# Kernel optimization log

Measured on AMD Instinct MI355X. Metric: run time of the kernel, lower is better.

Reference implementation:

```python
import jax, jax.numpy as jnp
import numpy as np

NUM_LEVELS = 4
RADIUS = 4


def avg_pool2(x):
    # x: [N, H, W] -> [N, H//2, W//2] (kernel 2, stride 2 average pool)
    n, h, w = x.shape
    return x.reshape(n, h // 2, 2, w // 2, 2).mean(axis=(2, 4))


def bilinear_sample(img, x, y):
    # img: [N, H, W]; x, y: [N, S, S] absolute pixel coords (align_corners=True),
    # zero padding outside [0, W-1] x [0, H-1] (matches F.grid_sample defaults).
    n, h, w = img.shape
    x0 = jnp.floor(x)
    y0 = jnp.floor(y)
    wx1 = x - x0
    wy1 = y - y0
    wx0 = 1.0 - wx1
    wy0 = 1.0 - wy1
    nidx = jnp.arange(n)[:, None, None]

    def gather(yi, xi):
        valid = (xi >= 0) & (xi <= w - 1) & (yi >= 0) & (yi <= h - 1)
        xic = jnp.clip(xi, 0, w - 1).astype(jnp.int32)
        yic = jnp.clip(yi, 0, h - 1).astype(jnp.int32)
        return jnp.where(valid, img[nidx, yic, xic], 0.0)

    return (gather(y0, x0) * wy0 * wx0 + gather(y0, x0 + 1) * wy0 * wx1
            + gather(y0 + 1, x0) * wy1 * wx0 + gather(y0 + 1, x0 + 1) * wy1 * wx1)


def setup_inputs() -> dict:
    key = jax.random.key(0)
    k1, k2, k3 = jax.random.split(key, 3)
    b, c, h, w = 2, 256, 64, 64
    fmap1 = jax.random.normal(k1, (b, c, h, w), dtype=jnp.float32)
    fmap2 = jax.random.normal(k2, (b, c, h, w), dtype=jnp.float32)
    # absolute pixel (x, y) coordinates in [0, W-1] / [0, H-1]
    centroids_coords = jax.random.uniform(k3, (b, 2, h, w), dtype=jnp.float32) * (w - 1)
    return {"fmap1": fmap1, "fmap2": fmap2, "centroids_coords": centroids_coords}


def reference(fmap1, fmap2, centroids_coords):
    b, c, h1, w1 = fmap1.shape
    h2, w2 = fmap2.shape[-2:]
    # correlation volume: [b, h1*w1, h2*w2] / sqrt(c)
    f1 = fmap1.reshape(b, c, h1 * w1)
    f2 = fmap2.reshape(b, c, h2 * w2)
    corr = jnp.einsum('bcm,bcn->bmn', f1, f2) / jnp.sqrt(jnp.asarray(c, fmap1.dtype))
    corr = corr.reshape(b * h1 * w1, h2, w2)

    pyramid = [corr]
    for _ in range(NUM_LEVELS - 1):
        corr = avg_pool2(corr)
        pyramid.append(corr)

    side = 2 * RADIUS + 1
    di = jnp.linspace(-RADIUS, RADIUS, side)
    # delta[..., 0] = di (added to x), delta[..., 1] = dj (added to y) -- as in source
    delta = jnp.stack(jnp.meshgrid(di, di, indexing='ij'), axis=-1)  # [S, S, 2]

    cc = centroids_coords.transpose(0, 2, 3, 1).reshape(b * h1 * w1, 1, 1, 2)
    feats = []
    for lvl, vol in enumerate(pyramid):
        grid = cc / (2.0 ** lvl) + delta[None]  # [N, S, S, 2]
        sampled = bilinear_sample(vol, grid[..., 0], grid[..., 1])  # [N, S, S]
        feats.append(sampled.reshape(b, h1, w1, side * side))
    # [b, num_levels*side^2, h1, w1]
    return jnp.concatenate(feats, axis=-1).transpose(0, 3, 1, 2)
```

## Files before the change

### kernel.cpp

```cpp
#include <hip/hip_runtime.h>
#include <stdint.h>

#define M_DIM 4096
#define K_DIM 256

typedef unsigned short us;
typedef __attribute__((ext_vector_type(8))) short bf16x8;
typedef __attribute__((ext_vector_type(4))) float f32x4;

static __device__ __forceinline__ float bf2f(unsigned int u){
  unsigned int x = u << 16; float f;
  __builtin_memcpy(&f, &x, 4); return f;
}
static __device__ __forceinline__ us f2bf(float f){
  unsigned int x; __builtin_memcpy(&x, &f, 4);
  unsigned int r = x + 0x7fffu + ((x >> 16) & 1u);
  return (us)(r >> 16);
}
static __device__ __forceinline__ void gld16(const void* g, void* l){
  __builtin_amdgcn_global_load_lds(
      (const __attribute__((address_space(1))) unsigned int*)g,
      (__attribute__((address_space(3))) unsigned int*)l, 16, 0, 0);
}

__global__ void k_transpose_cast(const float* __restrict__ f1,
                                 const float* __restrict__ f2,
                                 us* __restrict__ A, us* __restrict__ B0){
  __shared__ float lds[64][65];
  int z = blockIdx.z;
  int b = z & 1, which = z >> 1;
  const float* in = which ? f2 : f1;
  us* out = which ? B0 : A;
  float scale = which ? 1.0f : 0.0625f;
  int c0 = blockIdx.y * 64, m0 = blockIdx.x * 64;
  const float* ib = in + (size_t)b * K_DIM * M_DIM;
  us* ob = out + (size_t)b * M_DIM * K_DIM;
  int t = threadIdx.x, r = t >> 6, j = t & 63;
#pragma unroll
  for (int k = 0; k < 16; k++)
    lds[r + k*4][j] = ib[(size_t)(c0 + r + k*4) * M_DIM + m0 + j];
  __syncthreads();
#pragma unroll
  for (int k = 0; k < 16; k++)
    ob[(size_t)(m0 + r + k*4) * K_DIM + c0 + j] = f2bf(lds[j][r + k*4] * scale);
}

__global__ void k_pool_all(const us* __restrict__ B0, us* __restrict__ B1,
                           us* __restrict__ B2, us* __restrict__ B3){
  int bid = blockIdx.x;
  us* dst; int wd, f;
  if (bid < 512)      { dst = B1; wd = 32; f = 2; }
  else if (bid < 640) { bid -= 512; dst = B2; wd = 16; f = 4; }
  else                { bid -= 640; dst = B3; wd = 8;  f = 8; }
  int t = threadIdx.x;
  int idx = bid * 4 + (t >> 6);
  int l = t & 63;
  int per = wd * wd;
  int b = idx / per, rem = idx - b * per;
  int y = rem / wd, x = rem - y * wd;
  const us* sb = B0 + (size_t)b * 4096 * K_DIM;
  float s0 = 0, s1 = 0, s2 = 0, s3 = 0;
  for (int dy = 0; dy < f; dy++)
    for (int dx = 0; dx < f; dx++){
      size_t off = ((size_t)(f*y + dy) * 64 + (f*x + dx)) * K_DIM + l * 4;
      uint2 v = *(const uint2*)(sb + off);
      s0 += bf2f(v.x & 0xffff); s1 += bf2f(v.x >> 16);
      s2 += bf2f(v.y & 0xffff); s3 += bf2f(v.y >> 16);
    }
  float inv = 1.0f / (float)(f * f);
  uint2 o;
  o.x = (unsigned)f2bf(s0*inv) | ((unsigned)f2bf(s1*inv) << 16);
  o.y = (unsigned)f2bf(s2*inv) | ((unsigned)f2bf(s3*inv) << 16);
  us* db = dst + (size_t)b * per * K_DIM;
  *(uint2*)(db + (size_t)rem * K_DIM + l * 4) = o;
}

__global__ __launch_bounds__(256) void k_gemm_all(
    const us* __restrict__ A,
    const us* __restrict__ B0, const us* __restrict__ B1,
    const us* __restrict__ B2, const us* __restrict__ B3,
    us* __restrict__ C0, us* __restrict__ C1,
    us* __restrict__ C2, us* __restrict__ C3){
  __shared__ __align__(16) us As[2][4096];
  __shared__ __align__(16) us Bs[2][4096];
  int bx = blockIdx.x;
  const us* B; us* C; int N, n0;
  if (bx < 32)      { B = B0; C = C0; N = 4096; n0 = bx * 128; }
  else if (bx < 40) { B = B1; C = C1; N = 1024; n0 = (bx - 32) * 128; }
  else if (bx < 42) { B = B2; C = C2; N = 256;  n0 = (bx - 40) * 128; }
  else              { B = B3; C = C3; N = 64;   n0 = 0; }
  int b = blockIdx.z;
  const us* Ab = A + (size_t)b * M_DIM * K_DIM;
  const us* Bb = B + (size_t)b * N * K_DIM;
  us* Cb = C + (size_t)b * M_DIM * N;
  int m0 = blockIdx.y * 128;
  int t = threadIdx.x;
  int wave = t >> 6, lane = t & 63;
  int wm = (wave >> 1) * 64, wn = (wave & 1) * 64;
  int srow = t >> 2, scol = (t & 3) * 8;
  int fr = lane & 15, fk = (lane >> 4) * 8;
  f32x4 acc[4][4];
#pragma unroll
  for (int i = 0; i < 4; i++)
#pragma unroll
    for (int j = 0; j < 4; j++) acc[i][j] = (f32x4){0.f, 0.f, 0.f, 0.f};

  int nr0 = n0 + srow;      if (nr0 > N - 1) nr0 = N - 1;
  int nr1 = n0 + srow + 64; if (nr1 > N - 1) nr1 = N - 1;
  const us* ga0 = Ab + (size_t)(m0 + srow) * K_DIM + scol;
  const us* ga1 = Ab + (size_t)(m0 + srow + 64) * K_DIM + scol;
  const us* gb0 = Bb + (size_t)nr0 * K_DIM + scol;
  const us* gb1 = Bb + (size_t)nr1 * K_DIM + scol;

  gld16(ga0, &As[0][t*8]);
  gld16(ga1, &As[0][t*8 + 2048]);
  gld16(gb0, &Bs[0][t*8]);
  gld16(gb1, &Bs[0][t*8 + 2048]);
  asm volatile("s_waitcnt vmcnt(0)" ::: "memory");
  __syncthreads();

  int cur = 0;
  for (int it = 0; it < 8; ++it){
    if (it < 7){
      int kt = (it + 1) * 32;
      gld16(ga0 + kt, &As[cur^1][t*8]);
      gld16(ga1 + kt, &As[cur^1][t*8 + 2048]);
      gld16(gb0 + kt, &Bs[cur^1][t*8]);
      gld16(gb1 + kt, &Bs[cur^1][t*8 + 2048]);
    }
    bf16x8 af[4], bfv[4];
#pragma unroll
    for (int i = 0; i < 4; i++)
      af[i] = *(const bf16x8*)&As[cur][(wm + i*16 + fr) * 32 + fk];
#pragma unroll
    for (int j = 0; j < 4; j++)
      bfv[j] = *(const bf16x8*)&Bs[cur][(wn + j*16 + fr) * 32 + fk];
#pragma unroll
    for (int i = 0; i < 4; i++)
#pragma unroll
      for (int j = 0; j < 4; j++)
        acc[i][j] = __builtin_amdgcn_mfma_f32_16x16x32_bf16(af[i], bfv[j], acc[i][j], 0, 0, 0);
    asm volatile("s_waitcnt vmcnt(0)" ::: "memory");
    __syncthreads();
    cur ^= 1;
  }

  int cr = (lane >> 4) * 4, ccol = lane & 15;
#pragma unroll
  for (int i = 0; i < 4; i++){
#pragma unroll
    for (int j = 0; j < 4; j++){
      int col = n0 + wn + j*16 + ccol;
      if (col < N){
        size_t base = (size_t)(m0 + wm + i*16 + cr) * N + col;
#pragma unroll
        for (int r = 0; r < 4; r++)
          Cb[base + (size_t)r * N] = f2bf(acc[i][j][r]);
      }
    }
  }
}

__global__ __launch_bounds__(512) void k_sample(
    const us* __restrict__ p0, const us* __restrict__ p1,
    const us* __restrict__ p2, const us* __restrict__ p3,
    const float* __restrict__ cc, float* __restrict__ out){
  int i = blockIdx.x, b = blockIdx.y, lvl = blockIdx.z;
  int t = threadIdx.x;
  int w = t >> 6, j = t & 63;
  const us* corr; int wl;
  if (lvl == 0)      { corr = p0; wl = 64; }
  else if (lvl == 1) { corr = p1; wl = 32; }
  else if (lvl == 2) { corr = p2; wl = 16; }
  else               { corr = p3; wl = 8;  }
  float inv = 1.0f / (float)(1 << lvl);
  int m = i * 64 + j;
  const us* rowp = corr + (size_t)(b * M_DIM + m) * (wl * wl);
  float cx = cc[((size_t)(b*2 + 0) * 64 + i) * 64 + j];
  float cy = cc[((size_t)(b*2 + 1) * 64 + i) * 64 + j];
  float x = cx * inv, y = cy * inv;
  float x0f = floorf(x), y0f = floorf(y);
  int x0 = (int)x0f, y0 = (int)y0f;
  float fx = x - x0f, fy = y - y0f;

  int d_lo  = (w == 0) ? 0 : w + 1;
  int d_cnt = (w == 0) ? 2 : 1;
  int nrows = d_cnt + 1;

  int bxi = x0 - 4;
  int a0 = bxi & ~1;
  int par = bxi & 1;

  float Cw[3][12];
#pragma unroll
  for (int v = 0; v < 3; v++){
    int ry = y0 - 4 + d_lo + v;
    bool vy = ((unsigned)ry < (unsigned)wl) && (v < nrows);
    int ryc = ry < 0 ? 0 : (ry > wl - 1 ? wl - 1 : ry);
    const us* rp = rowp + ryc * wl;
#pragma unroll
    for (int k = 0; k < 6; k++){
      int e = a0 + 2*k;
      int ec = e < 0 ? 0 : (e > wl - 2 ? wl - 2 : e);
      unsigned dv = *(const unsigned*)(rp + ec);
      Cw[v][2*k]   = vy ? bf2f(dv & 0xffff) : 0.0f;
      Cw[v][2*k+1] = vy ? bf2f(dv >> 16)    : 0.0f;
    }
  }
  float T[3][10];
#pragma unroll
  for (int v = 0; v < 3; v++)
#pragma unroll
    for (int u = 0; u < 10; u++){
      float val = par ? Cw[v][u+1] : Cw[v][u];
      bool vx = (unsigned)(bxi + u) < (unsigned)wl;
      T[v][u] = vx ? val : 0.0f;
    }

  float wx1 = fx, wx0 = 1.0f - fx, wy1 = fy, wy0 = 1.0f - fy;
  size_t ob = (size_t)b * 324 + lvl * 81;
#pragma unroll
  for (int dd = 0; dd < 2; dd++){
    if (dd < d_cnt){
      int d = d_lo + dd;
#pragma unroll
      for (int a = 0; a < 9; a++){
        float val = wy0 * (wx0 * T[dd][a]   + wx1 * T[dd][a+1])
                  + wy1 * (wx0 * T[dd+1][a] + wx1 * T[dd+1][a+1]);
        out[((ob + a*9 + d) * 64 + i) * 64 + j] = val;
      }
    }
  }
}

extern "C" void kernel_launch(void* const* d_in, const int* in_sizes, int n_in,
                              void* d_out, int out_size, void* d_ws, size_t ws_size,
                              hipStream_t stream){
  (void)in_sizes; (void)n_in; (void)out_size; (void)ws_size;
  const float* f1 = (const float*)d_in[0];
  const float* f2 = (const float*)d_in[1];
  const float* cc = (const float*)d_in[2];
  float* out = (float*)d_out;
  char* ws = (char*)d_ws;
  us* A  = (us*)(ws + 0);
  us* B0 = (us*)(ws + 4194304);
  us* B1 = (us*)(ws + 8388608);
  us* B2 = (us*)(ws + 9437184);
  us* B3 = (us*)(ws + 9699328);
  us* C0 = (us*)(ws + 9764864);
  us* C1 = (us*)(ws + 76873728);
  us* C2 = (us*)(ws + 93650944);
  us* C3 = (us*)(ws + 97845248);

  k_transpose_cast<<<dim3(64, 4, 4), dim3(256), 0, stream>>>(f1, f2, A, B0);
  k_pool_all<<<dim3(672), dim3(256), 0, stream>>>(B0, B1, B2, B3);
  k_gemm_all<<<dim3(43, 32, 2), dim3(256), 0, stream>>>(A, B0, B1, B2, B3, C0, C1, C2, C3);
  k_sample<<<dim3(64, 2, 4), dim3(512), 0, stream>>>(C0, C1, C2, C3, cc, out);
}
```

Baseline: 160.7 us.

## Compute only the sampled correlation windows instead of the full correlation volume

Replaces the full all-pairs correlation GEMM and the separate sampling kernel with one fused kernel. Each wave handles one pixel and one pyramid level. It uses MFMA to compute dot products between that pixel's fmap1 feature and only the 10x10 neighbourhood of pooled fmap2 features, then does the bilinear interpolation from LDS. This relies on average pooling commuting with the dot product. It removes the large GEMM and the write and read of the tens-of-megabytes bf16 correlation volume. In exchange it does scattered row gathers from the pooled fmap2 buffers, and only one MFMA column out of sixteen is useful.

```diff
diff --git a/kernel.cpp b/kernel.cpp
--- a/kernel.cpp
+++ b/kernel.cpp
@@ -16,11 +16,6 @@
   unsigned int x; __builtin_memcpy(&x, &f, 4);
   unsigned int r = x + 0x7fffu + ((x >> 16) & 1u);
   return (us)(r >> 16);
-}
-static __device__ __forceinline__ void gld16(const void* g, void* l){
-  __builtin_amdgcn_global_load_lds(
-      (const __attribute__((address_space(1))) unsigned int*)g,
-      (__attribute__((address_space(3))) unsigned int*)l, 16, 0, 0);
 }
 
 __global__ void k_transpose_cast(const float* __restrict__ f1,
@@ -75,160 +70,82 @@
   *(uint2*)(db + (size_t)rem * K_DIM + l * 4) = o;
 }
 
-__global__ __launch_bounds__(256) void k_gemm_all(
+__global__ __launch_bounds__(256) void k_corrsample(
     const us* __restrict__ A,
     const us* __restrict__ B0, const us* __restrict__ B1,
     const us* __restrict__ B2, const us* __restrict__ B3,
-    us* __restrict__ C0, us* __restrict__ C1,
-    us* __restrict__ C2, us* __restrict__ C3){
-  __shared__ __align__(16) us As[2][4096];
-  __shared__ __align__(16) us Bs[2][4096];
-  int bx = blockIdx.x;
-  const us* B; us* C; int N, n0;
-  if (bx < 32)      { B = B0; C = C0; N = 4096; n0 = bx * 128; }
-  else if (bx < 40) { B = B1; C = C1; N = 1024; n0 = (bx - 32) * 128; }
-  else if (bx < 42) { B = B2; C = C2; N = 256;  n0 = (bx - 40) * 128; }
-  else              { B = B3; C = C3; N = 64;   n0 = 0; }
-  int b = blockIdx.z;
-  const us* Ab = A + (size_t)b * M_DIM * K_DIM;
-  const us* Bb = B + (size_t)b * N * K_DIM;
-  us* Cb = C + (size_t)b * M_DIM * N;
-  int m0 = blockIdx.y * 128;
-  int t = threadIdx.x;
-  int wave = t >> 6, lane = t & 63;
-  int wm = (wave >> 1) * 64, wn = (wave & 1) * 64;
-  int srow = t >> 2, scol = (t & 3) * 8;
-  int fr = lane & 15, fk = (lane >> 4) * 8;
-  f32x4 acc[4][4];
+    const float* __restrict__ cc, float* __restrict__ out){
+  __shared__ float tlds[4][112];
+  int wv = threadIdx.x >> 6, lane = threadIdx.x & 63;
+  int px = blockIdx.x;
+  int lvl = wv;
+  int b = px >> 12, m = px & 4095;
+  int i = m >> 6, j = m & 63;
+
+  const us* Bl; int wl;
+  if (lvl == 0)      { Bl = B0 + (size_t)b * 4096 * K_DIM; wl = 64; }
+  else if (lvl == 1) { Bl = B1 + (size_t)b * 1024 * K_DIM; wl = 32; }
+  else if (lvl == 2) { Bl = B2 + (size_t)b * 256  * K_DIM; wl = 16; }
+  else               { Bl = B3 + (size_t)b * 64   * K_DIM; wl = 8;  }
+  float inv = (lvl == 0) ? 1.0f : (lvl == 1) ? 0.5f : (lvl == 2) ? 0.25f : 0.125f;
+
+  float cx = cc[((size_t)(b*2 + 0) * 64 + i) * 64 + j];
+  float cy = cc[((size_t)(b*2 + 1) * 64 + i) * 64 + j];
+  float xs = cx * inv, ys = cy * inv;
+  float x0f = floorf(xs), y0f = floorf(ys);
+  int bx0 = (int)x0f - 4, by0 = (int)y0f - 4;
+  float fx = xs - x0f, fy = ys - y0f;
+
+  const us* f1p = A + (size_t)px * K_DIM;
+  int ko = (lane >> 4) * 8;
+  bf16x8 fB[8];
 #pragma unroll
-  for (int i = 0; i < 4; i++)
+  for (int kk = 0; kk < 8; kk++)
+    fB[kk] = *(const bf16x8*)(f1p + kk*32 + ko);
+
 #pragma unroll
-    for (int j = 0; j < 4; j++) acc[i][j] = (f32x4){0.f, 0.f, 0.f, 0.f};
-
-  int nr0 = n0 + srow;      if (nr0 > N - 1) nr0 = N - 1;
-  int nr1 = n0 + srow + 64; if (nr1 > N - 1) nr1 = N - 1;
-  const us* ga0 = Ab + (size_t)(m0 + srow) * K_DIM + scol;
-  const us* ga1 = Ab + (size_t)(m0 + srow + 64) * K_DIM + scol;
-  const us* gb0 = Bb + (size_t)nr0 * K_DIM + scol;
-  const us* gb1 = Bb + (size_t)nr1 * K_DIM + scol;
-
-  gld16(ga0, &As[0][t*8]);
-  gld16(ga1, &As[0][t*8 + 2048]);
-  gld16(gb0, &Bs[0][t*8]);
-  gld16(gb1, &Bs[0][t*8 + 2048]);
-  asm volatile("s_waitcnt vmcnt(0)" ::: "memory");
-  __syncthreads();
-
-  int cur = 0;
-  for (int it = 0; it < 8; ++it){
-    if (it < 7){
-      int kt = (it + 1) * 32;
-      gld16(ga0 + kt, &As[cur^1][t*8]);
-      gld16(ga1 + kt, &As[cur^1][t*8 + 2048]);
-      gld16(gb0 + kt, &Bs[cur^1][t*8]);
-      gld16(gb1 + kt, &Bs[cur^1][t*8 + 2048]);
+  for (int g = 0; g < 7; g++){
+    int tt = g*16 + (lane & 15);
+    int vv = (tt * 205) >> 11;
+    int uu = tt - vv * 10;
+    int ry = by0 + vv, rx = bx0 + uu;
+    int ryc = ry < 0 ? 0 : (ry > wl-1 ? wl-1 : ry);
+    int rxc = rx < 0 ? 0 : (rx > wl-1 ? wl-1 : rx);
+    const us* rowp = Bl + (size_t)(ryc * wl + rxc) * K_DIM;
+    f32x4 acc = (f32x4){0.f, 0.f, 0.f, 0.f};
+#pragma unroll
+    for (int kk = 0; kk < 8; kk++){
+      bf16x8 fA = *(const bf16x8*)(rowp + kk*32 + ko);
+      acc = __builtin_amdgcn_mfma_f32_16x16x32_bf16(fA, fB[kk], acc, 0, 0, 0);
     }
-    bf16x8 af[4], bfv[4];
+    int rbase = (lane >> 4) * 4;
+    float vals[4];
 #pragma unroll
-    for (int i = 0; i < 4; i++)
-      af[i] = *(const bf16x8*)&As[cur][(wm + i*16 + fr) * 32 + fk];
-#pragma unroll
-    for (int j = 0; j < 4; j++)
-      bfv[j] = *(const bf16x8*)&Bs[cur][(wn + j*16 + fr) * 32 + fk];
-#pragma unroll
-    for (int i = 0; i < 4; i++)
-#pragma unroll
-      for (int j = 0; j < 4; j++)
-        acc[i][j] = __builtin_amdgcn_mfma_f32_16x16x32_bf16(af[i], bfv[j], acc[i][j], 0, 0, 0);
-    asm volatile("s_waitcnt vmcnt(0)" ::: "memory");
-    __syncthreads();
-    cur ^= 1;
+    for (int rr = 0; rr < 4; rr++){
+      int tr = g*16 + rbase + rr;
+      int vr = (tr * 205) >> 11;
+      int ur = tr - vr * 10;
+      int ryr = by0 + vr, rxr = bx0 + ur;
+      bool ok = ((unsigned)ryr < (unsigned)wl) && ((unsigned)rxr < (unsigned)wl)
+                && (tr < 100);
+      vals[rr] = ok ? acc[rr] : 0.0f;
+    }
+    if ((lane & 15) == 0){
+      float4 v4; v4.x = vals[0]; v4.y = vals[1]; v4.z = vals[2]; v4.w = vals[3];
+      *(float4*)&tlds[wv][g*16 + rbase] = v4;
+    }
   }
 
-  int cr = (lane >> 4) * 4, ccol = lane & 15;
+  float wx1 = fx, wx0 = 1.0f - fx, wy1 = fy, wy0 = 1.0f - fy;
 #pragma unroll
-  for (int i = 0; i < 4; i++){
-#pragma unroll
-    for (int j = 0; j < 4; j++){
-      int col = n0 + wn + j*16 + ccol;
-      if (col < N){
-        size_t base = (size_t)(m0 + wm + i*16 + cr) * N + col;
-#pragma unroll
-        for (int r = 0; r < 4; r++)
-          Cb[base + (size_t)r * N] = f2bf(acc[i][j][r]);
-      }
-    }
-  }
-}
-
-__global__ __launch_bounds__(512) void k_sample(
-    const us* __restrict__ p0, const us* __restrict__ p1,
-    const us* __restrict__ p2, const us* __restrict__ p3,
-    const float* __restrict__ cc, float* __restrict__ out){
-  int i = blockIdx.x, b = blockIdx.y, lvl = blockIdx.z;
-  int t = threadIdx.x;
-  int w = t >> 6, j = t & 63;
-  const us* corr; int wl;
-  if (lvl == 0)      { corr = p0; wl = 64; }
-  else if (lvl == 1) { corr = p1; wl = 32; }
-  else if (lvl == 2) { corr = p2; wl = 16; }
-  else               { corr = p3; wl = 8;  }
-  float inv = 1.0f / (float)(1 << lvl);
-  int m = i * 64 + j;
-  const us* rowp = corr + (size_t)(b * M_DIM + m) * (wl * wl);
-  float cx = cc[((size_t)(b*2 + 0) * 64 + i) * 64 + j];
-  float cy = cc[((size_t)(b*2 + 1) * 64 + i) * 64 + j];
-  float x = cx * inv, y = cy * inv;
-  float x0f = floorf(x), y0f = floorf(y);
-  int x0 = (int)x0f, y0 = (int)y0f;
-  float fx = x - x0f, fy = y - y0f;
-
-  int d_lo  = (w == 0) ? 0 : w + 1;
-  int d_cnt = (w == 0) ? 2 : 1;
-  int nrows = d_cnt + 1;
-
-  int bxi = x0 - 4;
-  int a0 = bxi & ~1;
-  int par = bxi & 1;
-
-  float Cw[3][12];
-#pragma unroll
-  for (int v = 0; v < 3; v++){
-    int ry = y0 - 4 + d_lo + v;
-    bool vy = ((unsigned)ry < (unsigned)wl) && (v < nrows);
-    int ryc = ry < 0 ? 0 : (ry > wl - 1 ? wl - 1 : ry);
-    const us* rp = rowp + ryc * wl;
-#pragma unroll
-    for (int k = 0; k < 6; k++){
-      int e = a0 + 2*k;
-      int ec = e < 0 ? 0 : (e > wl - 2 ? wl - 2 : e);
-      unsigned dv = *(const unsigned*)(rp + ec);
-      Cw[v][2*k]   = vy ? bf2f(dv & 0xffff) : 0.0f;
-      Cw[v][2*k+1] = vy ? bf2f(dv >> 16)    : 0.0f;
-    }
-  }
-  float T[3][10];
-#pragma unroll
-  for (int v = 0; v < 3; v++)
-#pragma unroll
-    for (int u = 0; u < 10; u++){
-      float val = par ? Cw[v][u+1] : Cw[v][u];
-      bool vx = (unsigned)(bxi + u) < (unsigned)wl;
-      T[v][u] = vx ? val : 0.0f;
-    }
-
-  float wx1 = fx, wx0 = 1.0f - fx, wy1 = fy, wy0 = 1.0f - fy;
-  size_t ob = (size_t)b * 324 + lvl * 81;
-#pragma unroll
-  for (int dd = 0; dd < 2; dd++){
-    if (dd < d_cnt){
-      int d = d_lo + dd;
-#pragma unroll
-      for (int a = 0; a < 9; a++){
-        float val = wy0 * (wx0 * T[dd][a]   + wx1 * T[dd][a+1])
-                  + wy1 * (wx0 * T[dd+1][a] + wx1 * T[dd+1][a+1]);
-        out[((ob + a*9 + d) * 64 + i) * 64 + j] = val;
-      }
+  for (int rep = 0; rep < 2; rep++){
+    int o = lane + rep * 64;
+    if (o < 81){
+      int a = o / 9, d = o - a * 9;
+      int t0 = d * 10 + a;
+      float s = wy0 * (wx0 * tlds[wv][t0]      + wx1 * tlds[wv][t0 + 1])
+              + wy1 * (wx0 * tlds[wv][t0 + 10] + wx1 * tlds[wv][t0 + 11]);
+      out[(((size_t)b * 324 + lvl * 81 + o) * 64 + i) * 64 + j] = s;
     }
   }
 }
@@ -247,13 +164,8 @@
   us* B1 = (us*)(ws + 8388608);
   us* B2 = (us*)(ws + 9437184);
   us* B3 = (us*)(ws + 9699328);
-  us* C0 = (us*)(ws + 9764864);
-  us* C1 = (us*)(ws + 76873728);
-  us* C2 = (us*)(ws + 93650944);
-  us* C3 = (us*)(ws + 97845248);
 
   k_transpose_cast<<<dim3(64, 4, 4), dim3(256), 0, stream>>>(f1, f2, A, B0);
   k_pool_all<<<dim3(672), dim3(256), 0, stream>>>(B0, B1, B2, B3);
-  k_gemm_all<<<dim3(43, 32, 2), dim3(256), 0, stream>>>(A, B0, B1, B2, B3, C0, C1, C2, C3);
-  k_sample<<<dim3(64, 2, 4), dim3(512), 0, stream>>>(C0, C1, C2, C3, cc, out);
+  k_corrsample<<<dim3(8192), dim3(256), 0, stream>>>(A, B0, B1, B2, B3, cc, out);
 }
```

Result: slower. 286.4 us (+78.2%).

## Single-buffer GEMM staging and restructure sampler to wave-per-pixel with LDS transpose

Applied to the files above, without the earlier changes.

The GEMM drops double-buffered LDS staging in favour of a simple load, wait, compute loop with one buffer, which halves LDS use but serialises loads and MFMA work. The sampling kernel is rewritten so each wave handles one query pixel at a time. Each wave cooperatively loads the 10x12 window into LDS, computes all 81 outputs, and stages results in a shared tile before coalesced stores. The aim is coalesced reads of the correlation rows and better output writes, at the cost of serial rounds and LDS traffic. There is no barrier between Wt writes and reads within a wave, so correctness relies on lockstep execution within a wave.

```diff
diff --git a/kernel.cpp b/kernel.cpp
--- a/kernel.cpp
+++ b/kernel.cpp
@@ -81,8 +81,8 @@
     const us* __restrict__ B2, const us* __restrict__ B3,
     us* __restrict__ C0, us* __restrict__ C1,
     us* __restrict__ C2, us* __restrict__ C3){
-  __shared__ __align__(16) us As[2][4096];
-  __shared__ __align__(16) us Bs[2][4096];
+  __shared__ __align__(16) us As[4096];
+  __shared__ __align__(16) us Bs[4096];
   int bx = blockIdx.x;
   const us* B; us* C; int N, n0;
   if (bx < 32)      { B = B0; C = C0; N = 4096; n0 = bx * 128; }
@@ -112,37 +112,26 @@
   const us* gb0 = Bb + (size_t)nr0 * K_DIM + scol;
   const us* gb1 = Bb + (size_t)nr1 * K_DIM + scol;
 
-  gld16(ga0, &As[0][t*8]);
-  gld16(ga1, &As[0][t*8 + 2048]);
-  gld16(gb0, &Bs[0][t*8]);
-  gld16(gb1, &Bs[0][t*8 + 2048]);
-  asm volatile("s_waitcnt vmcnt(0)" ::: "memory");
-  __syncthreads();
-
-  int cur = 0;
-  for (int it = 0; it < 8; ++it){
-    if (it < 7){
-      int kt = (it + 1) * 32;
-      gld16(ga0 + kt, &As[cur^1][t*8]);
-      gld16(ga1 + kt, &As[cur^1][t*8 + 2048]);
-      gld16(gb0 + kt, &Bs[cur^1][t*8]);
-      gld16(gb1 + kt, &Bs[cur^1][t*8 + 2048]);
-    }
+  for (int kt = 0; kt < K_DIM; kt += 32){
+    __syncthreads();
+    gld16(ga0 + kt, As + t * 8);
+    gld16(ga1 + kt, As + t * 8 + 2048);
+    gld16(gb0 + kt, Bs + t * 8);
+    gld16(gb1 + kt, Bs + t * 8 + 2048);
+    asm volatile("s_waitcnt vmcnt(0)" ::: "memory");
+    __syncthreads();
     bf16x8 af[4], bfv[4];
 #pragma unroll
     for (int i = 0; i < 4; i++)
-      af[i] = *(const bf16x8*)&As[cur][(wm + i*16 + fr) * 32 + fk];
+      af[i] = *(const bf16x8*)(As + (wm + i*16 + fr) * 32 + fk);
 #pragma unroll
     for (int j = 0; j < 4; j++)
-      bfv[j] = *(const bf16x8*)&Bs[cur][(wn + j*16 + fr) * 32 + fk];
+      bfv[j] = *(const bf16x8*)(Bs + (wn + j*16 + fr) * 32 + fk);
 #pragma unroll
     for (int i = 0; i < 4; i++)
 #pragma unroll
       for (int j = 0; j < 4; j++)
         acc[i][j] = __builtin_amdgcn_mfma_f32_16x16x32_bf16(af[i], bfv[j], acc[i][j], 0, 0, 0);
-    asm volatile("s_waitcnt vmcnt(0)" ::: "memory");
-    __syncthreads();
-    cur ^= 1;
   }
 
   int cr = (lane >> 4) * 4, ccol = lane & 15;
@@ -161,75 +150,69 @@
   }
 }
 
-__global__ __launch_bounds__(512) void k_sample(
+__global__ __launch_bounds__(256) void k_sample(
     const us* __restrict__ p0, const us* __restrict__ p1,
     const us* __restrict__ p2, const us* __restrict__ p3,
     const float* __restrict__ cc, float* __restrict__ out){
+  __shared__ float Wt[4][10][12];
+  __shared__ float St[81][65];
   int i = blockIdx.x, b = blockIdx.y, lvl = blockIdx.z;
-  int t = threadIdx.x;
-  int w = t >> 6, j = t & 63;
+  int t = threadIdx.x, wv = t >> 6, lane = t & 63;
   const us* corr; int wl;
   if (lvl == 0)      { corr = p0; wl = 64; }
   else if (lvl == 1) { corr = p1; wl = 32; }
   else if (lvl == 2) { corr = p2; wl = 16; }
   else               { corr = p3; wl = 8;  }
   float inv = 1.0f / (float)(1 << lvl);
-  int m = i * 64 + j;
-  const us* rowp = corr + (size_t)(b * M_DIM + m) * (wl * wl);
-  float cx = cc[((size_t)(b*2 + 0) * 64 + i) * 64 + j];
-  float cy = cc[((size_t)(b*2 + 1) * 64 + i) * 64 + j];
-  float x = cx * inv, y = cy * inv;
-  float x0f = floorf(x), y0f = floorf(y);
-  int x0 = (int)x0f, y0 = (int)y0f;
-  float fx = x - x0f, fy = y - y0f;
-
-  int d_lo  = (w == 0) ? 0 : w + 1;
-  int d_cnt = (w == 0) ? 2 : 1;
-  int nrows = d_cnt + 1;
-
-  int bxi = x0 - 4;
-  int a0 = bxi & ~1;
-  int par = bxi & 1;
-
-  float Cw[3][12];
-#pragma unroll
-  for (int v = 0; v < 3; v++){
-    int ry = y0 - 4 + d_lo + v;
-    bool vy = ((unsigned)ry < (unsigned)wl) && (v < nrows);
-    int ryc = ry < 0 ? 0 : (ry > wl - 1 ? wl - 1 : ry);
-    const us* rp = rowp + ryc * wl;
-#pragma unroll
-    for (int k = 0; k < 6; k++){
-      int e = a0 + 2*k;
-      int ec = e < 0 ? 0 : (e > wl - 2 ? wl - 2 : e);
-      unsigned dv = *(const unsigned*)(rp + ec);
-      Cw[v][2*k]   = vy ? bf2f(dv & 0xffff) : 0.0f;
-      Cw[v][2*k+1] = vy ? bf2f(dv >> 16)    : 0.0f;
-    }
-  }
-  float T[3][10];
-#pragma unroll
-  for (int v = 0; v < 3; v++)
-#pragma unroll
-    for (int u = 0; u < 10; u++){
-      float val = par ? Cw[v][u+1] : Cw[v][u];
-      bool vx = (unsigned)(bxi + u) < (unsigned)wl;
-      T[v][u] = vx ? val : 0.0f;
-    }
-
-  float wx1 = fx, wx0 = 1.0f - fx, wy1 = fy, wy0 = 1.0f - fy;
-  size_t ob = (size_t)b * 324 + lvl * 81;
-#pragma unroll
-  for (int dd = 0; dd < 2; dd++){
-    if (dd < d_cnt){
-      int d = d_lo + dd;
-#pragma unroll
-      for (int a = 0; a < 9; a++){
-        float val = wy0 * (wx0 * T[dd][a]   + wx1 * T[dd][a+1])
-                  + wy1 * (wx0 * T[dd+1][a] + wx1 * T[dd+1][a+1]);
-        out[((ob + a*9 + d) * 64 + i) * 64 + j] = val;
+  int v = lane / 6, k = lane - v * 6;
+
+  for (int rnd = 0; rnd < 16; rnd++){
+    int jj = rnd * 4 + wv;
+    int m = i * 64 + jj;
+    const us* rowp = corr + (size_t)(b * M_DIM + m) * (wl * wl);
+    float cx = cc[((size_t)(b*2 + 0) * 64 + i) * 64 + jj];
+    float cy = cc[((size_t)(b*2 + 1) * 64 + i) * 64 + jj];
+    float xs = cx * inv, ys = cy * inv;
+    float x0f = floorf(xs), y0f = floorf(ys);
+    int bx0 = (int)x0f - 4, by0 = (int)y0f - 4;
+    float fx = xs - x0f, fy = ys - y0f;
+    int e0 = bx0 & ~1, par = bx0 & 1;
+
+    if (lane < 60){
+      int ry = by0 + v;
+      bool rok = (unsigned)ry < (unsigned)wl;
+      int ryc = ry < 0 ? 0 : (ry > wl - 1 ? wl - 1 : ry);
+      int si = e0 + 2 * k;
+      int ec = si < 0 ? 0 : (si > wl - 2 ? wl - 2 : si);
+      unsigned dv = *(const unsigned*)(rowp + ryc * wl + ec);
+      float lo = (rok && (unsigned)si       < (unsigned)wl) ? bf2f(dv & 0xffff) : 0.0f;
+      float hi = (rok && (unsigned)(si + 1) < (unsigned)wl) ? bf2f(dv >> 16)    : 0.0f;
+      Wt[wv][v][2*k]     = lo;
+      Wt[wv][v][2*k + 1] = hi;
+    }
+    float wx1 = fx, wx0 = 1.0f - fx, wy1 = fy, wy0 = 1.0f - fy;
+#pragma unroll
+    for (int p = 0; p < 2; p++){
+      int o = lane + p * 64;
+      if (o < 81){
+        int a = o / 9, d = o - a * 9;
+        float t00 = Wt[wv][d][a + par];
+        float t01 = Wt[wv][d][a + par + 1];
+        float t10 = Wt[wv][d + 1][a + par];
+        float t11 = Wt[wv][d + 1][a + par + 1];
+        St[o][jj] = wy0 * (wx0 * t00 + wx1 * t01) + wy1 * (wx0 * t10 + wx1 * t11);
       }
     }
+  }
+
+  __syncthreads();
+  size_t ob = ((size_t)b * 324 + lvl * 81) * 4096 + (size_t)i * 64;
+  int oo = t >> 6, j = t & 63;
+#pragma unroll
+  for (int r = 0; r < 21; r++){
+    int o = oo + r * 4;
+    if (o < 81)
+      out[ob + (size_t)o * 4096 + j] = St[o][j];
   }
 }
 
@@ -255,5 +238,5 @@
   k_transpose_cast<<<dim3(64, 4, 4), dim3(256), 0, stream>>>(f1, f2, A, B0);
   k_pool_all<<<dim3(672), dim3(256), 0, stream>>>(B0, B1, B2, B3);
   k_gemm_all<<<dim3(43, 32, 2), dim3(256), 0, stream>>>(A, B0, B1, B2, B3, C0, C1, C2, C3);
-  k_sample<<<dim3(64, 2, 4), dim3(512), 0, stream>>>(C0, C1, C2, C3, cc, out);
-}
+  k_sample<<<dim3(64, 2, 4), dim3(256), 0, stream>>>(C0, C1, C2, C3, cc, out);
+}
```

Result: faster. 149.8 us (-6.8%).
